# Optimization experiments

Measured on AMD Instinct MI355X. Metric: run time of the kernel, lower is better.

## Reference

```python
import jax, jax.numpy as jnp
import numpy as np

B, S, D = 4, 2048, 256
H, RANK, DFF = 8, 8, 1024
DK = D // H
EPS = 1e-5


def _linear(x, W, b):
    # torch nn.Linear: y = x @ W.T + b, W shape (out, in)
    return jnp.einsum('bsd,od->bso', x, W) + b


def _layer_norm(x, g, b):
    mu = jnp.mean(x, axis=-1, keepdims=True)
    var = jnp.var(x, axis=-1, keepdims=True)
    return (x - mu) * jax.lax.rsqrt(var + EPS) * g + b


def setup_inputs() -> dict:
    key = jax.random.key(0)
    ks = jax.random.split(key, 20)
    r = RANK * H
    s = lambda fan_in: 1.0 / np.sqrt(fan_in)
    inp = {
        'x': jax.random.normal(ks[0], (B, S, D), jnp.float32),
        'Wq_down': jax.random.uniform(ks[1], (r, D), jnp.float32, -s(D), s(D)),
        'bq_down': jnp.zeros((r,), jnp.float32),
        'Wq_up': jax.random.uniform(ks[2], (D, r), jnp.float32, -s(r), s(r)),
        'bq_up': jnp.zeros((D,), jnp.float32),
        'Wk_down': jax.random.uniform(ks[3], (r, D), jnp.float32, -s(D), s(D)),
        'bk_down': jnp.zeros((r,), jnp.float32),
        'Wk_up': jax.random.uniform(ks[4], (D, r), jnp.float32, -s(r), s(r)),
        'bk_up': jnp.zeros((D,), jnp.float32),
        'Wv': jax.random.uniform(ks[5], (D, D), jnp.float32, -s(D), s(D)),
        'bv': jnp.zeros((D,), jnp.float32),
        'Wo': jax.random.uniform(ks[6], (D, D), jnp.float32, -s(D), s(D)),
        'bo': jnp.zeros((D,), jnp.float32),
        'ln_attn_g': jnp.ones((D,), jnp.float32),
        'ln_attn_b': jnp.zeros((D,), jnp.float32),
        'W_ff1': jax.random.uniform(ks[7], (DFF, D), jnp.float32, -s(D), s(D)),
        'b_ff1': jnp.zeros((DFF,), jnp.float32),
        'W_ff2': jax.random.uniform(ks[8], (D, DFF), jnp.float32, -s(DFF), s(DFF)),
        'b_ff2': jnp.zeros((D,), jnp.float32),
        'ln_blk_g': jnp.ones((D,), jnp.float32),
        'ln_blk_b': jnp.zeros((D,), jnp.float32),
    }
    return inp


def reference(x, Wq_down, bq_down, Wq_up, bq_up, Wk_down, bk_down, Wk_up, bk_up,
              Wv, bv, Wo, bo, ln_attn_g, ln_attn_b,
              W_ff1, b_ff1, W_ff2, b_ff2, ln_blk_g, ln_blk_b):
    # Low-rank Q/K: down-project to rank*H then up-project to D
    Q = _linear(_linear(x, Wq_down, bq_down), Wq_up, bq_up)
    K = _linear(_linear(x, Wk_down, bk_down), Wk_up, bk_up)
    V = _linear(x, Wv, bv)
    # (B,S,D) -> (B,H,S,DK)
    Q = Q.reshape(B, S, H, DK).transpose(0, 2, 1, 3)
    K = K.reshape(B, S, H, DK).transpose(0, 2, 1, 3)
    V = V.reshape(B, S, H, DK).transpose(0, 2, 1, 3)
    scale = 1.0 / np.sqrt(DK).astype(np.float32)
    scores = jnp.einsum('bhqd,bhkd->bhqk', Q, K) * scale
    attn = jax.nn.softmax(scores, axis=-1)
    context = jnp.einsum('bhqk,bhkd->bhqd', attn, V)
    context = context.transpose(0, 2, 1, 3).reshape(B, S, D)
    attn_out = _linear(context, Wo, bo)
    attn_out = _layer_norm(x + attn_out, ln_attn_g, ln_attn_b)
    # FFN: Linear -> GELU (exact erf, torch default) -> Linear
    h = jax.nn.gelu(_linear(attn_out, W_ff1, b_ff1), approximate=False)
    ff = _linear(h, W_ff2, b_ff2)
    return _layer_norm(attn_out + ff, ln_blk_g, ln_blk_b)
```

## Files before the change

### kernel.cpp

```cpp
#include <hip/hip_runtime.h>
#include <hip/hip_bf16.h>
#include <math.h>

#define NB 4
#define NS 2048
#define ND 256
#define NH 8
#define NDK 32
#define NDFF 1024
#define NROWS (NB * NS)
#define KC 4
#define KVB 64
#define KTILES (NS / KC / KVB)
#define QVLD 384

using short8 = __attribute__((ext_vector_type(8))) short;
using f32x4  = __attribute__((ext_vector_type(4))) float;

__device__ __forceinline__ unsigned short f2bf(float f) {
  union { float f; unsigned u; } v; v.f = f;
  unsigned r = v.u + 0x7fffu + ((v.u >> 16) & 1u);
  return (unsigned short)(r >> 16);
}
__device__ __forceinline__ float bf2f(unsigned short u) {
  union { unsigned u; float f; } v; v.u = ((unsigned)u) << 16;
  return v.f;
}
__device__ __forceinline__ unsigned cvt_pk_bf16(float lo, float hi) {
  unsigned r;
  asm("v_cvt_pk_bf16_f32 %0, %1, %2" : "=v"(r) : "v"(lo), "v"(hi));
  return r;
}
__device__ __forceinline__ void gl_lds16(const void* g, void* l) {
  __builtin_amdgcn_global_load_lds(
      (const __attribute__((address_space(1))) unsigned int*)g,
      (__attribute__((address_space(3))) unsigned int*)l, 16, 0, 0);
}

__global__ void cvt_batch(const float* s0, const float* s1, const float* s2,
                          const float* s3, const float* s4, const float* s5,
                          const float* s6, const float* s7,
                          unsigned short* d0, unsigned short* d1,
                          unsigned short* d2, unsigned short* d3,
                          unsigned short* d4, unsigned short* d5,
                          unsigned short* d6, unsigned short* d7,
                          int n0, int n1, int n2, int n3, int n4, int n5,
                          int n6, int n7) {
  const float* s; unsigned short* d; int n;
  switch (blockIdx.y) {
    case 0: s = s0; d = d0; n = n0; break;
    case 1: s = s1; d = d1; n = n1; break;
    case 2: s = s2; d = d2; n = n2; break;
    case 3: s = s3; d = d3; n = n3; break;
    case 4: s = s4; d = d4; n = n4; break;
    case 5: s = s5; d = d5; n = n5; break;
    case 6: s = s6; d = d6; n = n6; break;
    default: s = s7; d = d7; n = n7; break;
  }
  for (int i = (blockIdx.x * 256 + threadIdx.x) * 4; i < n; i += 256 * 256 * 4) {
    float4 v = *reinterpret_cast<const float4*>(s + i);
    ushort4 o;
    o.x = f2bf(v.x); o.y = f2bf(v.y); o.z = f2bf(v.z); o.w = f2bf(v.w);
    *reinterpret_cast<ushort4*>(d + i) = o;
  }
}

template <int BM, int BN, int ACT, int OBF, int RES, int DUAL, int AF32,
          int ACOMB>
__global__ __launch_bounds__(256)
void gemm_nt(const void* __restrict__ Araw, int lda,
             const unsigned short* __restrict__ W, int ldw,
             const float* __restrict__ bias, const float* __restrict__ bias2,
             int bsplit, const float* __restrict__ bias3, int bsplit2,
             const void* __restrict__ resid, void* __restrict__ outp,
             int K, int O,
             const void* A2, const unsigned short* W2,
             const float* biasB, void* outp2,
             const unsigned short* paccp, const float* plp) {
  constexpr int MFW = BM / 32;
  constexpr int NFW = BN / 32;
  __shared__ __align__(16) unsigned short lA[2][BM * 64];
  __shared__ __align__(16) unsigned short lB[2][BN * 64];
  const int tid = threadIdx.x, lane = tid & 63, wid = tid >> 6;
  const int wr = wid >> 1, wc = wid & 1;
  const int l15 = lane & 15, lg = lane >> 4;
  const int bm = blockIdx.x, bn = blockIdx.y;

  const void* Ap = Araw;
  const unsigned short* Wp = W;
  const float* biasp = bias;
  void* outpp = outp;
  if (DUAL && blockIdx.z) {
    Ap = A2; Wp = W2; outpp = outp2;
    if (DUAL == 1) biasp = biasB;
  }

  auto stage = [&](int k0, int buf) {
#pragma unroll
    for (int it = 0; it < BM / 32; ++it) {
      int c = it * 256 + tid;
      int row = c >> 3, cc = (c & 7) ^ (row & 7);
      if (ACOMB) {
        int g = k0 + cc * 8;
        int grow = bm * BM + row;
        int b = grow >> 11, q = grow & 2047;
        int h = g >> 5, d = g & 31;
        size_t base = ((size_t)(b * 8 + h) * 2048 + q) * 32 + d;
        size_t lbase = (size_t)(b * 8 + h) * 2048 + q;
        float o0 = 0, o1 = 0, o2 = 0, o3 = 0, o4 = 0, o5 = 0, o6 = 0, o7 = 0;
        float L = 0.0f;
#pragma unroll
        for (int c2 = 0; c2 < KC; ++c2) {
          short8 a8 = *reinterpret_cast<const short8*>(
              paccp + (size_t)c2 * 2097152 + base);
          o0 += bf2f((unsigned short)a8[0]);
          o1 += bf2f((unsigned short)a8[1]);
          o2 += bf2f((unsigned short)a8[2]);
          o3 += bf2f((unsigned short)a8[3]);
          o4 += bf2f((unsigned short)a8[4]);
          o5 += bf2f((unsigned short)a8[5]);
          o6 += bf2f((unsigned short)a8[6]);
          o7 += bf2f((unsigned short)a8[7]);
          L += plp[(size_t)c2 * 65536 + lbase];
        }
        float inv = 1.0f / L;
        uint4 w;
        w.x = cvt_pk_bf16(o0 * inv, o1 * inv);
        w.y = cvt_pk_bf16(o2 * inv, o3 * inv);
        w.z = cvt_pk_bf16(o4 * inv, o5 * inv);
        w.w = cvt_pk_bf16(o6 * inv, o7 * inv);
        *reinterpret_cast<uint4*>(&lA[buf][c * 8]) = w;
      } else if (AF32) {
        const float* src =
            (const float*)Ap + (size_t)(bm * BM + row) * lda + k0 + cc * 8;
        float4 v0 = *reinterpret_cast<const float4*>(src);
        float4 v1 = *reinterpret_cast<const float4*>(src + 4);
        uint4 w;
        w.x = cvt_pk_bf16(v0.x, v0.y);
        w.y = cvt_pk_bf16(v0.z, v0.w);
        w.z = cvt_pk_bf16(v1.x, v1.y);
        w.w = cvt_pk_bf16(v1.z, v1.w);
        *reinterpret_cast<uint4*>(&lA[buf][c * 8]) = w;
      } else {
        gl_lds16((const unsigned short*)Ap +
                     (size_t)(bm * BM + row) * lda + k0 + cc * 8,
                 &lA[buf][c * 8]);
      }
    }
#pragma unroll
    for (int it = 0; it < BN / 32; ++it) {
      int c = it * 256 + tid;
      int row = c >> 3, cc = (c & 7) ^ (row & 7);
      gl_lds16(Wp + (size_t)(bn * BN + row) * ldw + k0 + cc * 8,
               &lB[buf][c * 8]);
    }
  };

  f32x4 acc[MFW][NFW];
#pragma unroll
  for (int i = 0; i < MFW; ++i)
#pragma unroll
    for (int j = 0; j < NFW; ++j) acc[i][j] = (f32x4)0.0f;

  const int T = K >> 6;
  stage(0, 0);
  __syncthreads();
  for (int t = 0; t < T; ++t) {
    const int cur = t & 1;
    if (t + 1 < T) stage((t + 1) << 6, cur ^ 1);
#pragma unroll
    for (int kk = 0; kk < 2; ++kk) {
      short8 a[MFW], b[NFW];
#pragma unroll
      for (int mf = 0; mf < MFW; ++mf) {
        int row = wr * (BM / 2) + mf * 16 + l15;
        a[mf] = *reinterpret_cast<const short8*>(
            &lA[cur][row * 64 + (((kk * 4 + lg) ^ (l15 & 7)) << 3)]);
      }
#pragma unroll
      for (int nf = 0; nf < NFW; ++nf) {
        int row = wc * (BN / 2) + nf * 16 + l15;
        b[nf] = *reinterpret_cast<const short8*>(
            &lB[cur][row * 64 + (((kk * 4 + lg) ^ (l15 & 7)) << 3)]);
      }
#pragma unroll
      for (int mf = 0; mf < MFW; ++mf)
#pragma unroll
        for (int nf = 0; nf < NFW; ++nf)
          acc[mf][nf] = __builtin_amdgcn_mfma_f32_16x16x32_bf16(
              a[mf], b[nf], acc[mf][nf], 0, 0, 0);
    }
    __syncthreads();
  }

  const bool zhalf = (DUAL == 2) && blockIdx.z;
#pragma unroll
  for (int mf = 0; mf < MFW; ++mf)
#pragma unroll
    for (int nf = 0; nf < NFW; ++nf) {
      int col = bn * BN + wc * (BN / 2) + nf * 16 + l15;
      float bv;
      if (zhalf) bv = 0.0f;
      else if (bias3 && col >= bsplit2) bv = bias3[col - bsplit2];
      else if (bias2 && col >= bsplit) bv = bias2[col - bsplit];
      else bv = biasp[col];
#pragma unroll
      for (int i = 0; i < 4; ++i) {
        int row = bm * BM + wr * (BM / 2) + mf * 16 + lg * 4 + i;
        float v = acc[mf][nf][i] + bv;
        if (ACT == 1) v = 0.5f * v * (1.0f + erff(v * 0.70710678118654752f));
        if (RES == 1 && !zhalf)
          v += ((const float*)resid)[(size_t)row * O + col];
        else if (RES == 2 && !zhalf)
          v += bf2f(((const unsigned short*)resid)[(size_t)row * O + col]);
        if (OBF)
          ((unsigned short*)outpp)[(size_t)row * O + col] = f2bf(v);
        else
          ((float*)outpp)[(size_t)row * O + col] = v;
      }
    }
}

__global__ __launch_bounds__(256)
void attn_kernel(const unsigned short* __restrict__ Qb,
                 const unsigned short* __restrict__ Kb,
                 const unsigned short* __restrict__ qv,
                 unsigned short* __restrict__ pacc,
                 float* __restrict__ pl) {
  __shared__ __align__(16) unsigned short lK[2][KVB * 32];
  __shared__ __align__(16) unsigned short lVt[2][32 * 64];
  __shared__ __align__(16) unsigned short lP[4][16 * 64];
  const int tid = threadIdx.x, lane = tid & 63, wid = tid >> 6;
  const int l15 = lane & 15, lg = lane >> 4;
  const int bh = blockIdx.x, qt = blockIdx.y, kc = blockIdx.z;
  const int b = bh >> 3, h = bh & 7;
  const size_t headoff = (size_t)h * NDK;
  const int qbase = qt * 128 + wid * 32;
  const int kv0 = kc * (NS / KC);
  const float qscale = 0.25508686f;

  short8 aq[2];
#pragma unroll
  for (int r = 0; r < 2; ++r) {
    short8 v = *reinterpret_cast<const short8*>(
        Qb + (size_t)(b * NS + qbase + r * 16 + l15) * ND + headoff + lg * 8);
#pragma unroll
    for (int j = 0; j < 8; ++j)
      v[j] = (short)f2bf(bf2f((unsigned short)v[j]) * qscale);
    aq[r] = v;
  }
  short8 ones8;
#pragma unroll
  for (int j = 0; j < 8; ++j) ones8[j] = (short)0x3F80;

  const unsigned short* kptr =
      Kb + (size_t)(b * NS + kv0 + (tid >> 2)) * ND + headoff +
      (((tid & 3) ^ ((tid >> 3) & 3)) << 3);
  const int vd0 = (tid & 15) * 2, vb = tid >> 4;
  const unsigned short* vptr =
      qv + (size_t)(b * NS + kv0 + vb * 4) * QVLD + 128 + headoff + vd0;
  const int vbs = vb ^ ((((tid & 15) * 2 >> 1) & 7) << 1);

  auto writeV = [&](const unsigned* w, int buf) {
    unsigned lo0 = (w[0] & 0xffffu) | (w[1] << 16);
    unsigned lo1 = (w[2] & 0xffffu) | (w[3] << 16);
    unsigned hi0 = (w[0] >> 16) | (w[1] & 0xffff0000u);
    unsigned hi1 = (w[2] >> 16) | (w[3] & 0xffff0000u);
    *reinterpret_cast<uint2*>(&lVt[buf][vd0 * 64 + vbs * 4]) =
        make_uint2(lo0, lo1);
    *reinterpret_cast<uint2*>(&lVt[buf][(vd0 + 1) * 64 + vbs * 4]) =
        make_uint2(hi0, hi1);
  };

  f32x4 accT[2][2];
  f32x4 accL[2];
#pragma unroll
  for (int r = 0; r < 2; ++r) {
    accL[r] = (f32x4)0.0f;
#pragma unroll
    for (int d = 0; d < 2; ++d) accT[r][d] = (f32x4)0.0f;
  }

  unsigned vr[4];
  gl_lds16(kptr, &lK[0][tid * 8]);
#pragma unroll
  for (int u = 0; u < 4; ++u)
    vr[u] = *reinterpret_cast<const unsigned*>(vptr + (size_t)u * QVLD);
  writeV(vr, 0);
  __syncthreads();

  for (int kt = 0; kt < KTILES; ++kt) {
    const int cur = kt & 1, nxt = cur ^ 1;
    const bool pf = (kt + 1 < KTILES);
    if (pf) {
      kptr += (size_t)KVB * ND;
      vptr += (size_t)KVB * QVLD;
      gl_lds16(kptr, &lK[nxt][tid * 8]);
#pragma unroll
      for (int u = 0; u < 4; ++u)
        vr[u] = *reinterpret_cast<const unsigned*>(vptr + (size_t)u * QVLD);
    }

#pragma unroll
    for (int r = 0; r < 2; ++r) {
      f32x4 sT[4];
      __builtin_amdgcn_s_setprio(1);
#pragma unroll
      for (int t = 0; t < 4; ++t) {
        short8 bk = *reinterpret_cast<const short8*>(
            &lK[cur][(t * 16 + l15) * 32 + ((lg ^ ((l15 >> 1) & 3)) << 3)]);
        sT[t] = __builtin_amdgcn_mfma_f32_16x16x32_bf16(
            bk, aq[r], (f32x4)0.0f, 0, 0, 0);
      }
      __builtin_amdgcn_s_setprio(0);
#pragma unroll
      for (int t = 0; t < 4; ++t) {
        float p0 = __builtin_amdgcn_exp2f(sT[t][0]);
        float p1 = __builtin_amdgcn_exp2f(sT[t][1]);
        float p2 = __builtin_amdgcn_exp2f(sT[t][2]);
        float p3 = __builtin_amdgcn_exp2f(sT[t][3]);
        unsigned w0 = cvt_pk_bf16(p0, p1);
        unsigned w1 = cvt_pk_bf16(p2, p3);
        int blk = (t << 1) | (lg >> 1);
        *reinterpret_cast<uint2*>(
            &lP[wid][l15 * 64 + ((blk ^ (l15 & 7)) << 3) + ((lg & 1) << 2)]) =
            make_uint2(w0, w1);
      }
      __builtin_amdgcn_s_setprio(1);
#pragma unroll
      for (int kk = 0; kk < 2; ++kk) {
        short8 pa = *reinterpret_cast<const short8*>(
            &lP[wid][l15 * 64 + (((kk * 4 + lg) ^ (l15 & 7)) << 3)]);
        accL[r] = __builtin_amdgcn_mfma_f32_16x16x32_bf16(
            ones8, pa, accL[r], 0, 0, 0);
#pragma unroll
        for (int dt = 0; dt < 2; ++dt) {
          int row = dt * 16 + l15;
          int bb = ((kk * 4 + lg) << 1) ^ (((l15 >> 1) & 7) << 1);
          short8 bv = *reinterpret_cast<const short8*>(
              &lVt[cur][row * 64 + (bb << 2)]);
          accT[r][dt] = __builtin_amdgcn_mfma_f32_16x16x32_bf16(
              bv, pa, accT[r][dt], 0, 0, 0);
        }
      }
      __builtin_amdgcn_s_setprio(0);
    }

    if (pf) writeV(vr, nxt);
    __syncthreads();
  }

#pragma unroll
  for (int r = 0; r < 2; ++r) {
    int qg = qbase + r * 16 + l15;
    size_t rowbase = ((size_t)kc * 65536 + (size_t)bh * NS + qg) * 32;
#pragma unroll
    for (int dt = 0; dt < 2; ++dt) {
      unsigned w0 = cvt_pk_bf16(accT[r][dt][0], accT[r][dt][1]);
      unsigned w1 = cvt_pk_bf16(accT[r][dt][2], accT[r][dt][3]);
      *reinterpret_cast<uint2*>(&pacc[rowbase + dt * 16 + lg * 4]) =
          make_uint2(w0, w1);
    }
  }
  if (lane < 16) {
#pragma unroll
    for (int r = 0; r < 2; ++r) {
      int qg = qbase + r * 16 + l15;
      pl[(size_t)kc * 65536 + (size_t)bh * NS + qg] = accL[r][0];
    }
  }
}

__global__ __launch_bounds__(256)
void ln_res_kernel(const float* __restrict__ a, const float* bsrc,
                   const float* __restrict__ g, const float* __restrict__ be,
                   float* yf, unsigned short* yb) {
  int row = blockIdx.x * 4 + (threadIdx.x >> 6);
  int lane = threadIdx.x & 63;
  size_t off = (size_t)row * ND + lane * 4;
  float4 va = *reinterpret_cast<const float4*>(a + off);
  float v0 = va.x, v1 = va.y, v2 = va.z, v3 = va.w;
  if (bsrc) {
    float4 vb = *reinterpret_cast<const float4*>(bsrc + off);
    v0 += vb.x; v1 += vb.y; v2 += vb.z; v3 += vb.w;
  }
  float s = v0 + v1 + v2 + v3;
  float sq = v0 * v0 + v1 * v1 + v2 * v2 + v3 * v3;
#pragma unroll
  for (int o = 1; o < 64; o <<= 1) {
    s += __shfl_xor(s, o);
    sq += __shfl_xor(sq, o);
  }
  float mu = s * (1.0f / 256.0f);
  float var = sq * (1.0f / 256.0f) - mu * mu;
  float rs = rsqrtf(var + 1e-5f);
  float4 vg = *reinterpret_cast<const float4*>(g + lane * 4);
  float4 vbe = *reinterpret_cast<const float4*>(be + lane * 4);
  float o0 = (v0 - mu) * rs * vg.x + vbe.x;
  float o1 = (v1 - mu) * rs * vg.y + vbe.y;
  float o2 = (v2 - mu) * rs * vg.z + vbe.z;
  float o3 = (v3 - mu) * rs * vg.w + vbe.w;
  if (yf) *reinterpret_cast<float4*>(yf + off) = make_float4(o0, o1, o2, o3);
  if (yb) {
    ushort4 ob;
    ob.x = f2bf(o0); ob.y = f2bf(o1); ob.z = f2bf(o2); ob.w = f2bf(o3);
    *reinterpret_cast<ushort4*>(yb + off) = ob;
  }
}

extern "C" void kernel_launch(void* const* d_in, const int* in_sizes, int n_in,
                              void* d_out, int out_size, void* d_ws,
                              size_t ws_size, hipStream_t stream) {
  (void)in_sizes; (void)n_in; (void)out_size; (void)ws_size;
  const float* x   = (const float*)d_in[0];
  const float* Wqd = (const float*)d_in[1];
  const float* bqd = (const float*)d_in[2];
  const float* Wqu = (const float*)d_in[3];
  const float* bqu = (const float*)d_in[4];
  const float* Wkd = (const float*)d_in[5];
  const float* bkd = (const float*)d_in[6];
  const float* Wku = (const float*)d_in[7];
  const float* bku = (const float*)d_in[8];
  const float* Wv  = (const float*)d_in[9];
  const float* bv  = (const float*)d_in[10];
  const float* Wo  = (const float*)d_in[11];
  const float* bo  = (const float*)d_in[12];
  const float* g1  = (const float*)d_in[13];
  const float* be1 = (const float*)d_in[14];
  const float* Wf1 = (const float*)d_in[15];
  const float* bf1 = (const float*)d_in[16];
  const float* Wf2 = (const float*)d_in[17];
  const float* bf2 = (const float*)d_in[18];
  const float* g2  = (const float*)d_in[19];
  const float* be2 = (const float*)d_in[20];

  char* p = (char*)d_ws;
  auto alloc = [&](size_t bytes) {
    char* r = p;
    p += (bytes + 255) & ~(size_t)255;
    return r;
  };
  unsigned short* wqkv = (unsigned short*)alloc(384 * 256 * 2);
  unsigned short* wqu  = (unsigned short*)alloc(256 * 64 * 2);
  unsigned short* wku  = (unsigned short*)alloc(256 * 64 * 2);
  unsigned short* wo   = (unsigned short*)alloc(256 * 256 * 2);
  unsigned short* wf1  = (unsigned short*)alloc(1024 * 256 * 2);
  unsigned short* wf2  = (unsigned short*)alloc(256 * 1024 * 2);
  unsigned short* qv   = (unsigned short*)alloc((size_t)NROWS * QVLD * 2);
  unsigned short* Qb   = (unsigned short*)alloc((size_t)NROWS * ND * 2);
  unsigned short* Kb   = (unsigned short*)alloc((size_t)NROWS * ND * 2);
  float*          pl   = (float*)alloc((size_t)KC * 65536 * 4);
  unsigned short* y1b  = (unsigned short*)alloc((size_t)NROWS * ND * 2);
  float*          ao2  = (float*)alloc((size_t)NROWS * ND * 4);
  unsigned short* hb   = (unsigned short*)alloc((size_t)NROWS * NDFF * 2);
  float* ao = (float*)d_out;

  unsigned short* pacc = hb;

  cvt_batch<<<dim3(256, 8), 256, 0, stream>>>(
      Wqd, Wkd, Wqu, Wku, Wv, Wo, Wf1, Wf2,
      wqkv, wqkv + 64 * 256, wqu, wku, wqkv + 128 * 256, wo, wf1, wf2,
      64 * 256, 64 * 256, 256 * 64, 256 * 64, 256 * 256,
      256 * 256, 1024 * 256, 256 * 1024);

  gemm_nt<64, 64, 0, 1, 0, 0, 1, 0><<<dim3(128, 6), 256, 0, stream>>>(
      x, 256, wqkv, 256, bqd, bkd, 64, bv, 128, nullptr, qv, 256, QVLD,
      nullptr, nullptr, nullptr, nullptr, nullptr, nullptr);
  gemm_nt<64, 64, 0, 1, 0, 1, 0, 0><<<dim3(128, 4, 2), 256, 0, stream>>>(
      qv, QVLD, wqu, 64, bqu, nullptr, 0, nullptr, 0, nullptr, Qb, 64, 256,
      qv + 64, wku, bku, Kb, nullptr, nullptr);

  attn_kernel<<<dim3(NB * NH, NS / 128, KC), 256, 0, stream>>>(
      Qb, Kb, qv, pacc, pl);

  gemm_nt<64, 64, 0, 0, 1, 0, 0, 1><<<dim3(128, 4), 256, 0, stream>>>(
      nullptr, 256, wo, 256, bo, nullptr, 0, nullptr, 0, x, ao, 256, 256,
      nullptr, nullptr, nullptr, nullptr, pacc, pl);
  ln_res_kernel<<<NROWS / 4, 256, 0, stream>>>(ao, nullptr, g1, be1,
                                               nullptr, y1b);

  gemm_nt<128, 128, 1, 1, 0, 0, 0, 0><<<dim3(64, 8), 256, 0, stream>>>(
      y1b, 256, wf1, 256, bf1, nullptr, 0, nullptr, 0, nullptr, hb, 256, NDFF,
      nullptr, nullptr, nullptr, nullptr, nullptr, nullptr);
  gemm_nt<64, 64, 0, 0, 2, 2, 0, 0><<<dim3(128, 4, 2), 256, 0, stream>>>(
      hb, 1024, wf2, 1024, bf2, nullptr, 0, nullptr, 0, y1b, ao, 512, 256,
      hb + 512, wf2 + 512, nullptr, ao2, nullptr, nullptr);
  ln_res_kernel<<<NROWS / 4, 256, 0, stream>>>(ao, ao2, g2, be2,
                                               (float*)d_out, nullptr);
}
```

Before: 107.1 us.

## Keep softmax probabilities in registers and permute V layout to match MFMA fragments

Removes the per-wave LDS staging buffer for the probability tile. The exp2 results are packed straight into MFMA A-operands, and the V transposed tile in LDS is re-indexed with a matching permuted k-ordering so the register layout of P lines up with it. K fragments are also hoisted out of the row loop so they are read once per tile instead of once per row pair. This saves LDS writes, reads and their latency, but relies on the permuted V swizzle being correct and adds some register pressure.

```diff
diff --git a/kernel.cpp b/kernel.cpp
--- a/kernel.cpp
+++ b/kernel.cpp
@@ -229,7 +229,6 @@
                  float* __restrict__ pl) {
   __shared__ __align__(16) unsigned short lK[2][KVB * 32];
   __shared__ __align__(16) unsigned short lVt[2][32 * 64];
-  __shared__ __align__(16) unsigned short lP[4][16 * 64];
   const int tid = threadIdx.x, lane = tid & 63, wid = tid >> 6;
   const int l15 = lane & 15, lg = lane >> 4;
   const int bh = blockIdx.x, qt = blockIdx.y, kc = blockIdx.z;
@@ -256,19 +255,22 @@
   const unsigned short* kptr =
       Kb + (size_t)(b * NS + kv0 + (tid >> 2)) * ND + headoff +
       (((tid & 3) ^ ((tid >> 3) & 3)) << 3);
-  const int vd0 = (tid & 15) * 2, vb = tid >> 4;
+  const int vd0 = (tid & 15) * 2, vk0 = (tid >> 4) * 4;
   const unsigned short* vptr =
-      qv + (size_t)(b * NS + kv0 + vb * 4) * QVLD + 128 + headoff + vd0;
-  const int vbs = vb ^ ((((tid & 15) * 2 >> 1) & 7) << 1);
+      qv + (size_t)(b * NS + kv0 + vk0) * QVLD + 128 + headoff + vd0;
+  const int vB16 = (vk0 >> 5) * 4 + ((vk0 >> 2) & 3);
+  const int vhalf = (vk0 >> 4) & 1;
+  const int vsw = (vd0 >> 1) & 7;
+  const int vshort = (((vB16 ^ vsw) << 1) | vhalf) * 4;
 
   auto writeV = [&](const unsigned* w, int buf) {
     unsigned lo0 = (w[0] & 0xffffu) | (w[1] << 16);
     unsigned lo1 = (w[2] & 0xffffu) | (w[3] << 16);
     unsigned hi0 = (w[0] >> 16) | (w[1] & 0xffff0000u);
     unsigned hi1 = (w[2] >> 16) | (w[3] & 0xffff0000u);
-    *reinterpret_cast<uint2*>(&lVt[buf][vd0 * 64 + vbs * 4]) =
+    *reinterpret_cast<uint2*>(&lVt[buf][vd0 * 64 + vshort]) =
         make_uint2(lo0, lo1);
-    *reinterpret_cast<uint2*>(&lVt[buf][(vd0 + 1) * 64 + vbs * 4]) =
+    *reinterpret_cast<uint2*>(&lVt[buf][(vd0 + 1) * 64 + vshort]) =
         make_uint2(hi0, hi1);
   };
 
@@ -301,44 +303,45 @@
         vr[u] = *reinterpret_cast<const unsigned*>(vptr + (size_t)u * QVLD);
     }
 
+    short8 bk[4];
+#pragma unroll
+    for (int t = 0; t < 4; ++t)
+      bk[t] = *reinterpret_cast<const short8*>(
+          &lK[cur][(t * 16 + l15) * 32 + ((lg ^ ((l15 >> 1) & 3)) << 3)]);
+
 #pragma unroll
     for (int r = 0; r < 2; ++r) {
       f32x4 sT[4];
       __builtin_amdgcn_s_setprio(1);
 #pragma unroll
-      for (int t = 0; t < 4; ++t) {
-        short8 bk = *reinterpret_cast<const short8*>(
-            &lK[cur][(t * 16 + l15) * 32 + ((lg ^ ((l15 >> 1) & 3)) << 3)]);
+      for (int t = 0; t < 4; ++t)
         sT[t] = __builtin_amdgcn_mfma_f32_16x16x32_bf16(
-            bk, aq[r], (f32x4)0.0f, 0, 0, 0);
-      }
+            bk[t], aq[r], (f32x4)0.0f, 0, 0, 0);
       __builtin_amdgcn_s_setprio(0);
+      unsigned wv[4][2];
 #pragma unroll
       for (int t = 0; t < 4; ++t) {
         float p0 = __builtin_amdgcn_exp2f(sT[t][0]);
         float p1 = __builtin_amdgcn_exp2f(sT[t][1]);
         float p2 = __builtin_amdgcn_exp2f(sT[t][2]);
         float p3 = __builtin_amdgcn_exp2f(sT[t][3]);
-        unsigned w0 = cvt_pk_bf16(p0, p1);
-        unsigned w1 = cvt_pk_bf16(p2, p3);
-        int blk = (t << 1) | (lg >> 1);
-        *reinterpret_cast<uint2*>(
-            &lP[wid][l15 * 64 + ((blk ^ (l15 & 7)) << 3) + ((lg & 1) << 2)]) =
-            make_uint2(w0, w1);
+        wv[t][0] = cvt_pk_bf16(p0, p1);
+        wv[t][1] = cvt_pk_bf16(p2, p3);
       }
       __builtin_amdgcn_s_setprio(1);
 #pragma unroll
       for (int kk = 0; kk < 2; ++kk) {
-        short8 pa = *reinterpret_cast<const short8*>(
-            &lP[wid][l15 * 64 + (((kk * 4 + lg) ^ (l15 & 7)) << 3)]);
+        union { uint4 u; short8 s; } pc;
+        pc.u = make_uint4(wv[2 * kk][0], wv[2 * kk][1],
+                          wv[2 * kk + 1][0], wv[2 * kk + 1][1]);
+        short8 pa = pc.s;
         accL[r] = __builtin_amdgcn_mfma_f32_16x16x32_bf16(
             ones8, pa, accL[r], 0, 0, 0);
 #pragma unroll
         for (int dt = 0; dt < 2; ++dt) {
-          int row = dt * 16 + l15;
-          int bb = ((kk * 4 + lg) << 1) ^ (((l15 >> 1) & 7) << 1);
+          int B16r = (kk * 4 + lg) ^ ((l15 >> 1) & 7);
           short8 bv = *reinterpret_cast<const short8*>(
-              &lVt[cur][row * 64 + (bb << 2)]);
+              &lVt[cur][(dt * 16 + l15) * 64 + B16r * 8]);
           accT[r][dt] = __builtin_amdgcn_mfma_f32_16x16x32_bf16(
               bv, pa, accT[r][dt], 0, 0, 0);
         }
```

After: 103.9 us. 1.03x faster.
